# Performance work log

Hardware: AMD Instinct MI355X
Metric: run time of the kernel (lower is better)

The kernel has to match this reference:

```python
import jax, jax.numpy as jnp
import numpy as np


def setup_inputs() -> dict:
    key = jax.random.key(0)
    kq, kk, kv = jax.random.split(key, 3)
    B, H, N, D = 2, 16, 2048, 64
    q = jax.random.normal(kq, (B, H, N, D), dtype=jnp.float32)
    k = jax.random.normal(kk, (B, H, N, D), dtype=jnp.float32)
    v = jax.random.normal(kv, (B, H, N, D), dtype=jnp.float32)
    return {"q": q, "k": k, "v": v}


def reference(q, k, v):
    # RBF-kernel causal attention: logits = -relu(||q-k||^2) / sqrt(D)
    B, H, N, D = q.shape
    sm_scale = 1.0 / jnp.sqrt(jnp.asarray(D, dtype=q.dtype))
    q_sq = jnp.sum(q * q, axis=-1)              # [B,H,N]
    k_sq = jnp.sum(k * k, axis=-1)              # [B,H,N]
    qk = jnp.einsum("bhmd,bhnd->bhmn", q, k)    # [B,H,N,N]
    dist_sq = q_sq[..., :, None] + k_sq[..., None, :] - 2.0 * qk
    dist_sq = jnp.maximum(dist_sq, 0.0)         # relu on squared distance
    logits = -dist_sq * sm_scale
    # causal mask: query m attends to keys n <= m
    causal = jnp.tril(jnp.ones((N, N), dtype=bool))
    logits = jnp.where(causal, logits, -jnp.inf)
    p = jax.nn.softmax(logits, axis=-1)
    out = jnp.einsum("bhmn,bhnd->bhmd", p, v)
    return out
```

## Files before the change

### kernel.cpp

```cpp
#include <hip/hip_runtime.h>

#define NN 2048
#define DD 64
#define C1 0.36067376f
#define C1H 0.18033688f

typedef _Float16 h8 __attribute__((ext_vector_type(8)));
typedef _Float16 h4 __attribute__((ext_vector_type(4)));
typedef float f32x16 __attribute__((ext_vector_type(16)));

union H8U4 { h8 v; unsigned u[4]; };

static __device__ inline float max3f(float a, float b, float c) {
    return fmaxf(fmaxf(a, b), c);
}

static __device__ inline float ph_max(float v) {
    unsigned u; __builtin_memcpy(&u, &v, 4);
    auto rr = __builtin_amdgcn_permlane32_swap(u, u, false, false);
    unsigned r0 = rr[0], r1 = rr[1];
    float a, b; __builtin_memcpy(&a, &r0, 4); __builtin_memcpy(&b, &r1, 4);
    return fmaxf(a, b);
}
static __device__ inline float ph_sum(float v) {
    unsigned u; __builtin_memcpy(&u, &v, 4);
    auto rr = __builtin_amdgcn_permlane32_swap(u, u, false, false);
    unsigned r0 = rr[0], r1 = rr[1];
    float a, b; __builtin_memcpy(&a, &r0, 4); __builtin_memcpy(&b, &r1, 4);
    return a + b;
}

__global__ __launch_bounds__(64) void prep(const float* __restrict__ k,
                                           const float* __restrict__ v,
                                           _Float16* __restrict__ Ks,
                                           _Float16* __restrict__ Vs,
                                           float* __restrict__ hk) {
    __shared__ _Float16 T[32][72];
    const int jj = blockIdx.x, bh = blockIdx.y, lane = threadIdx.x;
    const int ln = lane & 31, lh = lane >> 5;
    const size_t ibase = (size_t)bh * NN * DD + (size_t)jj * 32 * DD;

    {
        const float* kr = k + ibase + (size_t)ln * DD;
        float s = 0.f;
#pragma unroll
        for (int c = 0; c < 4; ++c) {
            float4 a = *(const float4*)&kr[16 * c + 8 * lh];
            float4 b = *(const float4*)&kr[16 * c + 8 * lh + 4];
            h8 o = {(_Float16)a.x, (_Float16)a.y, (_Float16)a.z, (_Float16)a.w,
                    (_Float16)b.x, (_Float16)b.y, (_Float16)b.z, (_Float16)b.w};
            *(h8*)&Ks[((size_t)bh * 16384 + jj * 256 + c * 64 + lh * 32 + ln) * 8] = o;
            s += a.x*a.x + a.y*a.y + a.z*a.z + a.w*a.w
               + b.x*b.x + b.y*b.y + b.z*b.z + b.w*b.w;
        }
        s += __shfl_xor(s, 32);
        if (lh == 0) hk[bh * NN + jj * 32 + ln] = s * (-C1H);
    }

#pragma unroll
    for (int t = 0; t < 8; ++t) {
        int f = lane + 64 * t;
        int row = f >> 4, c4 = (f & 15) * 4;
        float4 a = *(const float4*)&v[ibase + (size_t)row * DD + c4];
        h4 hv = {(_Float16)a.x, (_Float16)a.y, (_Float16)a.z, (_Float16)a.w};
        *(h4*)&T[row][c4] = hv;
    }
    __syncthreads();
#pragma unroll
    for (int oc = 0; oc < 4; ++oc) {
        int o = oc >> 1, c = oc & 1;
        h8 r;
#pragma unroll
        for (int jx = 0; jx < 8; ++jx) r[jx] = T[16 * c + 8 * lh + jx][32 * o + ln];
        *(h8*)&Vs[((size_t)bh * 16384 + jj * 256 + o * 128 + c * 64 + lh * 32 + ln) * 8] = r;
    }
}

__global__ __launch_bounds__(128, 2) void rbf_attn(
    const float* __restrict__ q, const _Float16* __restrict__ Ks,
    const _Float16* __restrict__ Vs, const float* __restrict__ hk,
    float* __restrict__ out)
{
    __shared__ float sm[64][34];
    const int tid = threadIdx.x;
    const int n = blockIdx.x;
    const int bh = (n & 7) * 4 + ((n >> 3) & 3);
    const int qt = 63 - (n >> 5);
    const int wv = tid >> 6, lane = tid & 63;
    const int ln = lane & 31, lh = lane >> 5;
    const int qrow = qt * 32 + ln;
    const size_t fbase = (size_t)bh * NN * DD;

    h8 qf[4];
    {
        const float* qr = q + fbase + (size_t)qrow * DD;
#pragma unroll
        for (int c = 0; c < 4; ++c) {
            float4 a = *(const float4*)&qr[16 * c + 8 * lh];
            float4 b = *(const float4*)&qr[16 * c + 8 * lh + 4];
            qf[c] = h8{(_Float16)(C1 * a.x), (_Float16)(C1 * a.y),
                       (_Float16)(C1 * a.z), (_Float16)(C1 * a.w),
                       (_Float16)(C1 * b.x), (_Float16)(C1 * b.y),
                       (_Float16)(C1 * b.z), (_Float16)(C1 * b.w)};
        }
    }

    const _Float16* Ksb = Ks + (size_t)bh * 131072;
    const _Float16* Vsb = Vs + (size_t)bh * 131072;
    const float4* hk4 = (const float4*)(hk + bh * NN);
    const int klq = (lh * 32 + ln) * 8;

    f32x16 O0, O1;
#pragma unroll
    for (int r = 0; r < 16; ++r) { O0[r] = 0.f; O1[r] = 0.f; }
    float lsum = 0.f, mrun = -INFINITY;

    const int T = qt + 1;
    const int half = (T + 1) >> 1;
    const int j0 = wv ? half : 0;
    const int j1 = wv ? T : half;

    auto loadKH = [&](int jj, h8 (&kf)[4], float4 (&hr)[4]) {
        const _Float16* kp = Ksb + (size_t)jj * 2048 + klq;
#pragma unroll
        for (int c = 0; c < 4; ++c) kf[c] = *(const h8*)(kp + c * 512);
#pragma unroll
        for (int g = 0; g < 4; ++g) hr[g] = hk4[jj * 8 + g * 2 + lh];
    };
    auto loadV = [&](int jj, h8 (&vf)[4]) {
        const _Float16* vp = Vsb + (size_t)jj * 2048 + klq;
#pragma unroll
        for (int oc = 0; oc < 4; ++oc)
            vf[oc] = *(const h8*)(vp + (oc >> 1) * 1024 + (oc & 1) * 512);
    };

    auto qk = [&](const h8 (&kf)[4], const float4 (&hr)[4]) {
        f32x16 S;
#pragma unroll
        for (int r = 0; r < 16; ++r) S[r] = ((const float*)&hr[r >> 2])[r & 3];
#pragma unroll
        for (int c = 0; c < 4; ++c)
            S = __builtin_amdgcn_mfma_f32_32x32x16_f16(kf[c], qf[c], S, 0, 0, 0);
        return S;
    };

    auto smpv = [&](int jj, const f32x16& S, const h8 (&vf)[4]) {
        const bool diag = (jj == qt);
        float x[16];
#pragma unroll
        for (int r = 0; r < 16; ++r) {
            float xv = S[r];
            if (diag) {
                int keyloc = (r & 3) + 8 * (r >> 2) + 4 * lh;
                if (keyloc > ln) xv = -INFINITY;
            }
            x[r] = xv;
        }
        float m0 = max3f(x[0], x[1], x[2]);
        float m1 = max3f(x[3], x[4], x[5]);
        float m2 = max3f(x[6], x[7], x[8]);
        float m3 = max3f(x[9], x[10], x[11]);
        float m4 = max3f(x[12], x[13], x[14]);
        float mt = max3f(max3f(m0, m1, m2), fmaxf(m3, m4), x[15]);
        mt = ph_max(mt);
        float mnew = fmaxf(mrun, mt);
        float alpha = __builtin_amdgcn_exp2f(mrun - mnew);
        mrun = mnew;
        float p[16], ps;
#pragma unroll
        for (int r = 0; r < 16; ++r) p[r] = __builtin_amdgcn_exp2f(x[r] - mnew);
        ps = (((p[0] + p[1]) + (p[2] + p[3])) + ((p[4] + p[5]) + (p[6] + p[7])))
           + (((p[8] + p[9]) + (p[10] + p[11])) + ((p[12] + p[13]) + (p[14] + p[15])));
        lsum = fmaf(lsum, alpha, ps);
#pragma unroll
        for (int r = 0; r < 16; ++r) { O0[r] *= alpha; O1[r] *= alpha; }

        unsigned pk[8];
#pragma unroll
        for (int hh = 0; hh < 8; ++hh) {
            auto prr = __builtin_amdgcn_cvt_pkrtz(p[2 * hh], p[2 * hh + 1]);
            unsigned pu; __builtin_memcpy(&pu, &prr, 4);
            pk[hh] = pu;
        }
#pragma unroll
        for (int s = 0; s < 2; ++s) {
            auto r02 = __builtin_amdgcn_permlane32_swap(pk[4 * s + 0], pk[4 * s + 2],
                                                        false, false);
            auto r13 = __builtin_amdgcn_permlane32_swap(pk[4 * s + 1], pk[4 * s + 3],
                                                        false, false);
            H8U4 pb;
            pb.u[0] = r02[0];
            pb.u[1] = r13[0];
            pb.u[2] = r02[1];
            pb.u[3] = r13[1];
            O0 = __builtin_amdgcn_mfma_f32_32x32x16_f16(vf[s], pb.v, O0, 0, 0, 0);
            O1 = __builtin_amdgcn_mfma_f32_32x32x16_f16(vf[2 + s], pb.v, O1, 0, 0, 0);
        }
    };

    if (j0 < j1) {
        h8 kfA[4], kfB[4], vfA[4], vfB[4];
        float4 hrA[4], hrB[4];
        loadKH(j0, kfA, hrA);
        loadV(j0, vfA);
        int jp = (j0 + 1 < j1) ? j0 + 1 : j1 - 1;
        loadKH(jp, kfB, hrB);
        f32x16 Sa = qk(kfA, hrA);
        f32x16 Sb;
        int jj = j0;
        while (true) {
            Sb = qk(kfB, hrB);
            { int jn = (jj + 1 < j1) ? jj + 1 : j1 - 1; loadV(jn, vfB); }
            { int jn = (jj + 2 < j1) ? jj + 2 : j1 - 1; loadKH(jn, kfA, hrA); }
            smpv(jj, Sa, vfA);
            if (++jj >= j1) break;
            Sa = qk(kfA, hrA);
            { int jn = (jj + 1 < j1) ? jj + 1 : j1 - 1; loadV(jn, vfA); }
            { int jn = (jj + 2 < j1) ? jj + 2 : j1 - 1; loadKH(jn, kfB, hrB); }
            smpv(jj, Sb, vfB);
            if (++jj >= j1) break;
        }
    }

    if (wv) {
#pragma unroll
        for (int r = 0; r < 16; ++r) { sm[lane][r] = O0[r]; sm[lane][16 + r] = O1[r]; }
        sm[lane][32] = ph_sum(lsum);
        sm[lane][33] = mrun;
    }
    __syncthreads();
    if (!wv) {
        float l0 = ph_sum(lsum);
        float l1 = sm[lane][32];
        float m1 = sm[lane][33];
        float m = fmaxf(mrun, m1);
        float a0 = __builtin_amdgcn_exp2f(mrun - m);
        float a1 = __builtin_amdgcn_exp2f(m1 - m);
        float lt = l0 * a0 + l1 * a1;
        float inv = 1.f / lt;
        float s0 = a0 * inv, s1 = a1 * inv;
        size_t ro = fbase + (size_t)qrow * DD;
#pragma unroll
        for (int g = 0; g < 4; ++g) {
            float4 o0 = make_float4(O0[4 * g + 0] * s0 + sm[lane][4 * g + 0] * s1,
                                    O0[4 * g + 1] * s0 + sm[lane][4 * g + 1] * s1,
                                    O0[4 * g + 2] * s0 + sm[lane][4 * g + 2] * s1,
                                    O0[4 * g + 3] * s0 + sm[lane][4 * g + 3] * s1);
            *(float4*)&out[ro + 8 * g + 4 * lh] = o0;
            float4 o1 = make_float4(O1[4 * g + 0] * s0 + sm[lane][16 + 4 * g + 0] * s1,
                                    O1[4 * g + 1] * s0 + sm[lane][16 + 4 * g + 1] * s1,
                                    O1[4 * g + 2] * s0 + sm[lane][16 + 4 * g + 2] * s1,
                                    O1[4 * g + 3] * s0 + sm[lane][16 + 4 * g + 3] * s1);
            *(float4*)&out[ro + 32 + 8 * g + 4 * lh] = o1;
        }
    }
}

extern "C" void kernel_launch(void* const* d_in, const int* in_sizes, int n_in,
                              void* d_out, int out_size, void* d_ws, size_t ws_size,
                              hipStream_t stream) {
    (void)in_sizes; (void)n_in; (void)out_size; (void)ws_size;
    const float* q = (const float*)d_in[0];
    const float* k = (const float*)d_in[1];
    const float* v = (const float*)d_in[2];
    float* out = (float*)d_out;

    float* hk = (float*)d_ws;
    _Float16* Ks = (_Float16*)((char*)d_ws + 262144);
    _Float16* Vs = (_Float16*)((char*)d_ws + 262144 + 8388608);

    prep<<<dim3(64, 32), 64, 0, stream>>>(k, v, Ks, Vs, hk);
    rbf_attn<<<dim3(2048), 128, 0, stream>>>(q, Ks, Vs, hk, out);
}
```

Measured before the change: 127.8 us.

## Fold key-norm bias into an extra MFMA and drop LDS transpose in prep

```diff
diff --git a/kernel.cpp b/kernel.cpp
--- a/kernel.cpp
+++ b/kernel.cpp
@@ -6,10 +6,10 @@
 #define C1H 0.18033688f
 
 typedef _Float16 h8 __attribute__((ext_vector_type(8)));
-typedef _Float16 h4 __attribute__((ext_vector_type(4)));
 typedef float f32x16 __attribute__((ext_vector_type(16)));
 
 union H8U4 { h8 v; unsigned u[4]; };
+union HU { _Float16 h; unsigned short b; };
 
 static __device__ inline float max3f(float a, float b, float c) {
     return fmaxf(fmaxf(a, b), c);
@@ -30,13 +30,15 @@
     return a + b;
 }
 
-__global__ __launch_bounds__(64) void prep(const float* __restrict__ k,
-                                           const float* __restrict__ v,
-                                           _Float16* __restrict__ Ks,
-                                           _Float16* __restrict__ Vs,
-                                           float* __restrict__ hk) {
-    __shared__ _Float16 T[32][72];
-    const int jj = blockIdx.x, bh = blockIdx.y, lane = threadIdx.x;
+__global__ __launch_bounds__(256) void prep(const float* __restrict__ k,
+                                            const float* __restrict__ v,
+                                            _Float16* __restrict__ Ks,
+                                            _Float16* __restrict__ Vs,
+                                            unsigned* __restrict__ hk2) {
+    const int bx = blockIdx.x, bh = blockIdx.y;
+    const int tid = threadIdx.x;
+    const int wv = tid >> 6, lane = tid & 63;
+    const int jj = bx * 4 + wv;
     const int ln = lane & 31, lh = lane >> 5;
     const size_t ibase = (size_t)bh * NN * DD + (size_t)jj * 32 * DD;
 
@@ -54,31 +56,28 @@
                + b.x*b.x + b.y*b.y + b.z*b.z + b.w*b.w;
         }
         s += __shfl_xor(s, 32);
-        if (lh == 0) hk[bh * NN + jj * 32 + ln] = s * (-C1H);
-    }
-
-#pragma unroll
-    for (int t = 0; t < 8; ++t) {
-        int f = lane + 64 * t;
-        int row = f >> 4, c4 = (f & 15) * 4;
-        float4 a = *(const float4*)&v[ibase + (size_t)row * DD + c4];
-        h4 hv = {(_Float16)a.x, (_Float16)a.y, (_Float16)a.z, (_Float16)a.w};
-        *(h4*)&T[row][c4] = hv;
-    }
-    __syncthreads();
+        if (lh == 0) {
+            float vv = -C1H * s;
+            HU hi; hi.h = (_Float16)vv;
+            HU lo; lo.h = (_Float16)(vv - (float)hi.h);
+            hk2[bh * NN + jj * 32 + ln] = (unsigned)hi.b | ((unsigned)lo.b << 16);
+        }
+    }
+
 #pragma unroll
     for (int oc = 0; oc < 4; ++oc) {
         int o = oc >> 1, c = oc & 1;
+        const float* vb = v + ibase + (size_t)(16 * c + 8 * lh) * DD + 32 * o + ln;
         h8 r;
 #pragma unroll
-        for (int jx = 0; jx < 8; ++jx) r[jx] = T[16 * c + 8 * lh + jx][32 * o + ln];
+        for (int jx = 0; jx < 8; ++jx) r[jx] = (_Float16)vb[(size_t)jx * DD];
         *(h8*)&Vs[((size_t)bh * 16384 + jj * 256 + o * 128 + c * 64 + lh * 32 + ln) * 8] = r;
     }
 }
 
 __global__ __launch_bounds__(128, 2) void rbf_attn(
     const float* __restrict__ q, const _Float16* __restrict__ Ks,
-    const _Float16* __restrict__ Vs, const float* __restrict__ hk,
+    const _Float16* __restrict__ Vs, const unsigned* __restrict__ hk2,
     float* __restrict__ out)
 {
     __shared__ float sm[64][34];
@@ -92,6 +91,7 @@
     const size_t fbase = (size_t)bh * NN * DD;
 
     h8 qf[4];
+    H8U4 qc4;
     {
         const float* qr = q + fbase + (size_t)qrow * DD;
 #pragma unroll
@@ -103,11 +103,13 @@
                        (_Float16)(C1 * b.x), (_Float16)(C1 * b.y),
                        (_Float16)(C1 * b.z), (_Float16)(C1 * b.w)};
         }
+        qc4.u[0] = lh ? 0u : 0x3C003C00u;
+        qc4.u[1] = 0u; qc4.u[2] = 0u; qc4.u[3] = 0u;
     }
 
     const _Float16* Ksb = Ks + (size_t)bh * 131072;
     const _Float16* Vsb = Vs + (size_t)bh * 131072;
-    const float4* hk4 = (const float4*)(hk + bh * NN);
+    const unsigned* hk2b = hk2 + bh * NN;
     const int klq = (lh * 32 + ln) * 8;
 
     f32x16 O0, O1;
@@ -120,12 +122,11 @@
     const int j0 = wv ? half : 0;
     const int j1 = wv ? T : half;
 
-    auto loadKH = [&](int jj, h8 (&kf)[4], float4 (&hr)[4]) {
+    auto loadKB = [&](int jj, h8 (&kf)[4], unsigned& bias) {
         const _Float16* kp = Ksb + (size_t)jj * 2048 + klq;
 #pragma unroll
         for (int c = 0; c < 4; ++c) kf[c] = *(const h8*)(kp + c * 512);
-#pragma unroll
-        for (int g = 0; g < 4; ++g) hr[g] = hk4[jj * 8 + g * 2 + lh];
+        bias = hk2b[jj * 32 + ln];
     };
     auto loadV = [&](int jj, h8 (&vf)[4]) {
         const _Float16* vp = Vsb + (size_t)jj * 2048 + klq;
@@ -134,10 +135,14 @@
             vf[oc] = *(const h8*)(vp + (oc >> 1) * 1024 + (oc & 1) * 512);
     };
 
-    auto qk = [&](const h8 (&kf)[4], const float4 (&hr)[4]) {
+    auto qk = [&](const h8 (&kf)[4], unsigned bias) {
         f32x16 S;
 #pragma unroll
-        for (int r = 0; r < 16; ++r) S[r] = ((const float*)&hr[r >> 2])[r & 3];
+        for (int r = 0; r < 16; ++r) S[r] = 0.f;
+        H8U4 k4;
+        k4.u[0] = lh ? 0u : bias;
+        k4.u[1] = 0u; k4.u[2] = 0u; k4.u[3] = 0u;
+        S = __builtin_amdgcn_mfma_f32_32x32x16_f16(k4.v, qc4.v, S, 0, 0, 0);
 #pragma unroll
         for (int c = 0; c < 4; ++c)
             S = __builtin_amdgcn_mfma_f32_32x32x16_f16(kf[c], qf[c], S, 0, 0, 0);
@@ -200,23 +205,23 @@
 
     if (j0 < j1) {
         h8 kfA[4], kfB[4], vfA[4], vfB[4];
-        float4 hrA[4], hrB[4];
-        loadKH(j0, kfA, hrA);
+        unsigned biA, biB;
+        loadKB(j0, kfA, biA);
         loadV(j0, vfA);
         int jp = (j0 + 1 < j1) ? j0 + 1 : j1 - 1;
-        loadKH(jp, kfB, hrB);
-        f32x16 Sa = qk(kfA, hrA);
+        loadKB(jp, kfB, biB);
+        f32x16 Sa = qk(kfA, biA);
         f32x16 Sb;
         int jj = j0;
         while (true) {
-            Sb = qk(kfB, hrB);
+            Sb = qk(kfB, biB);
             { int jn = (jj + 1 < j1) ? jj + 1 : j1 - 1; loadV(jn, vfB); }
-            { int jn = (jj + 2 < j1) ? jj + 2 : j1 - 1; loadKH(jn, kfA, hrA); }
+            { int jn = (jj + 2 < j1) ? jj + 2 : j1 - 1; loadKB(jn, kfA, biA); }
             smpv(jj, Sa, vfA);
             if (++jj >= j1) break;
-            Sa = qk(kfA, hrA);
+            Sa = qk(kfA, biA);
             { int jn = (jj + 1 < j1) ? jj + 1 : j1 - 1; loadV(jn, vfA); }
-            { int jn = (jj + 2 < j1) ? jj + 2 : j1 - 1; loadKH(jn, kfB, hrB); }
+            { int jn = (jj + 2 < j1) ? jj + 2 : j1 - 1; loadKB(jn, kfB, biB); }
             smpv(jj, Sb, vfB);
             if (++jj >= j1) break;
         }
@@ -265,10 +270,10 @@
     const float* v = (const float*)d_in[2];
     float* out = (float*)d_out;
 
-    float* hk = (float*)d_ws;
+    unsigned* hk2 = (unsigned*)d_ws;
     _Float16* Ks = (_Float16*)((char*)d_ws + 262144);
     _Float16* Vs = (_Float16*)((char*)d_ws + 262144 + 8388608);
 
-    prep<<<dim3(64, 32), 64, 0, stream>>>(k, v, Ks, Vs, hk);
-    rbf_attn<<<dim3(2048), 128, 0, stream>>>(q, Ks, Vs, hk, out);
-}
+    prep<<<dim3(16, 32), 256, 0, stream>>>(k, v, Ks, Vs, hk2);
+    rbf_attn<<<dim3(2048), 128, 0, stream>>>(q, Ks, Vs, hk2, out);
+}
```

After: 127.3 us. No clear change (-0.3%).
